# Performance work log

Hardware: AMD Instinct MI355X
Metric: run time of the kernel (lower is better)

## Reference

```python
import jax, jax.numpy as jnp
import numpy as np

B, S, D, C, H = 4, 2048, 1024, 2, 16
LN_EPS = 1e-5


def setup_inputs() -> dict:
    key = jax.random.key(0)
    ks = jax.random.split(key, 6)
    return {
        "token_emb": jax.random.normal(ks[0], (B, S, D), dtype=jnp.float32),
        "chunk_w": jax.random.normal(ks[1], (D, C * D), dtype=jnp.float32) * 0.02,
        "chunk_b": jnp.zeros((D,), dtype=jnp.float32),
        "in_proj_w": jax.random.normal(ks[2], (3 * D, D), dtype=jnp.float32) * 0.02,
        "in_proj_b": jnp.zeros((3 * D,), dtype=jnp.float32),
        "out_proj_w": jax.random.normal(ks[3], (D, D), dtype=jnp.float32) * 0.02,
        "out_proj_b": jnp.zeros((D,), dtype=jnp.float32),
        "ln_g": jnp.ones((D,), dtype=jnp.float32),
        "ln_b": jnp.zeros((D,), dtype=jnp.float32),
        "num_heads": H,
    }


def _layer_norm(x, g, b):
    mu = jnp.mean(x, axis=-1, keepdims=True)
    var = jnp.mean((x - mu) ** 2, axis=-1, keepdims=True)
    return (x - mu) * jax.lax.rsqrt(var + LN_EPS) * g + b


def reference(token_emb, chunk_w, chunk_b, in_proj_w, in_proj_b,
              out_proj_w, out_proj_b, ln_g, ln_b, num_heads):
    Bq, Sq, Dq = token_emb.shape
    c = chunk_w.shape[1] // Dq
    # Sliding windows with zero padding at the end (vectorized unfold).
    padded = jnp.pad(token_emb, ((0, 0), (0, c - 1), (0, 0)))
    # (B, S, c*D): concat the c shifted views along feature dim
    windows = jnp.concatenate([padded[:, k:k + Sq, :] for k in range(c)], axis=-1)
    chunk = jnp.einsum('bsf,df->bsd', windows, chunk_w) + chunk_b  # (B,S,D)

    # Multi-head self-attention (torch nn.MultiheadAttention semantics).
    qkv = jnp.einsum('bsd,ed->bse', chunk, in_proj_w) + in_proj_b
    q, k, v = jnp.split(qkv, 3, axis=-1)
    dh = Dq // num_heads
    q = q.reshape(Bq, Sq, num_heads, dh)
    k = k.reshape(Bq, Sq, num_heads, dh)
    v = v.reshape(Bq, Sq, num_heads, dh)
    scores = jnp.einsum('bqhd,bkhd->bhqk', q, k) / jnp.sqrt(jnp.float32(dh))
    probs = jax.nn.softmax(scores, axis=-1)
    attn = jnp.einsum('bhqk,bkhd->bqhd', probs, v).reshape(Bq, Sq, Dq)
    attn = jnp.einsum('bsd,ed->bse', attn, out_proj_w) + out_proj_b

    return _layer_norm(chunk + attn, ln_g, ln_b)
```

## Files before the change

kernel.cpp:

```cpp
#include <hip/hip_runtime.h>


typedef __bf16 bf16x8 __attribute__((ext_vector_type(8)));
typedef float f32x4 __attribute__((ext_vector_type(4)));
typedef float f32x16 __attribute__((ext_vector_type(16)));

#if __has_builtin(__builtin_amdgcn_exp2f)
#define EXP2(x) __builtin_amdgcn_exp2f(x)
#else
#define EXP2(x) exp2f(x)
#endif

__device__ __forceinline__ unsigned short f2bf(float x) {
  unsigned u = __float_as_uint(x);
  u += 0x7fffu + ((u >> 16) & 1u);
  return (unsigned short)(u >> 16);
}

__device__ __forceinline__ float bf2f(unsigned short x) {
  return __uint_as_float(((unsigned)x) << 16);
}

__device__ __forceinline__ void glds16(const ushort* g, ushort* l) {
  __builtin_amdgcn_global_load_lds(
      (const __attribute__((address_space(1))) unsigned int*)g,
      (__attribute__((address_space(3))) unsigned int*)l, 16, 0, 0);
}

__global__ __launch_bounds__(256) void build_awin(const float* __restrict__ emb,
                                                  ushort* __restrict__ aw) {
  const int i = blockIdx.x * 256 + threadIdx.x;
  const int e = i * 4;
  const int m = e >> 11;
  const int k = e & 2047;
  float4 v;
  if (k < 1024) {
    v = *(const float4*)(emb + (size_t)m * 1024 + k);
  } else {
    const int s = m & 2047;
    if (s == 2047) v = make_float4(0.f, 0.f, 0.f, 0.f);
    else           v = *(const float4*)(emb + (size_t)(m + 1) * 1024 + (k - 1024));
  }
  ushort4 o;
  o.x = f2bf(v.x); o.y = f2bf(v.y); o.z = f2bf(v.z); o.w = f2bf(v.w);
  *(ushort4*)(aw + (size_t)e) = o;
}

__global__ __launch_bounds__(256) void cvt_bf16(const float* __restrict__ in,
                                                ushort* __restrict__ out, int n4) {
  const int i = blockIdx.x * 256 + threadIdx.x;
  if (i >= n4) return;
  float4 v = ((const float4*)in)[i];
  ushort4 o;
  o.x = f2bf(v.x); o.y = f2bf(v.y); o.z = f2bf(v.z); o.w = f2bf(v.w);
  ((ushort4*)out)[i] = o;
}

template <int NT>
__global__ __launch_bounds__(256) void gemm_bt(
    const ushort* __restrict__ A, const ushort* __restrict__ W,
    const float* __restrict__ bias, int M, int N, int K, int mode,
    float* __restrict__ outf, ushort* __restrict__ outb,
    const ushort* __restrict__ residb) {
  constexpr int NTC = NT / 32;
  constexpr int BC  = NT / 32;
  __shared__ __align__(16) ushort sA[8192];
  __shared__ __align__(16) ushort sB[NT * 64];
  const int t = threadIdx.x, wave = t >> 6, lane = t & 63;
  const int c16 = lane & 15, quad = lane >> 4;
  const int wm = wave >> 1, wn = wave & 1;
  const int m0 = blockIdx.x * 128, n0 = blockIdx.y * NT;
  f32x4 acc[4][NTC] = {};
  const ushort* gA[4];
  const ushort* gB[BC];
  ushort* lA[4];
  ushort* lB[BC];
#pragma unroll
  for (int c = 0; c < 4; ++c) {
    const int j = wave * 4 + c;
    const int ks = j >> 1, row = (j & 1) * 64 + lane;
    gA[c] = A + (size_t)(m0 + row) * K + ks * 8;
    lA[c] = sA + j * 512;
  }
#pragma unroll
  for (int c = 0; c < BC; ++c) {
    const int j = wave * BC + c;
    int ksb, rowb;
    if (NT == 128) { ksb = j >> 1; rowb = (j & 1) * 64 + lane; }
    else           { ksb = j;      rowb = lane; }
    gB[c] = W + (size_t)(n0 + rowb) * K + ksb * 8;
    lB[c] = sB + j * 512;
  }
  for (int k0 = 0; k0 < K; k0 += 64) {
    __syncthreads();
#pragma unroll
    for (int c = 0; c < 4; ++c) glds16(gA[c] + k0, lA[c]);
#pragma unroll
    for (int c = 0; c < BC; ++c) glds16(gB[c] + k0, lB[c]);
    __syncthreads();
#pragma unroll
    for (int kc = 0; kc < 2; ++kc) {
      bf16x8 af[4], bfr[NTC];
#pragma unroll
      for (int i = 0; i < 4; ++i)
        af[i] = *(const bf16x8*)(sA + ((kc * 4 + quad) * 128 + wm * 64 + i * 16 + c16) * 8);
#pragma unroll
      for (int i = 0; i < NTC; ++i)
        bfr[i] = *(const bf16x8*)(sB + ((kc * 4 + quad) * NT + wn * (NT / 2) + i * 16 + c16) * 8);
#pragma unroll
      for (int mt = 0; mt < 4; ++mt)
#pragma unroll
        for (int nt = 0; nt < NTC; ++nt)
          acc[mt][nt] = __builtin_amdgcn_mfma_f32_16x16x32_bf16(af[mt], bfr[nt],
                                                                acc[mt][nt], 0, 0, 0);
    }
  }
  const float QS = 0.18033688011112042f;
  float bv[NTC];
#pragma unroll
  for (int nt = 0; nt < NTC; ++nt) bv[nt] = bias[n0 + wn * (NT / 2) + nt * 16 + c16];
#pragma unroll
  for (int mt = 0; mt < 4; ++mt) {
#pragma unroll
    for (int nt = 0; nt < NTC; ++nt) {
      const int n = n0 + wn * (NT / 2) + nt * 16 + c16;
#pragma unroll
      for (int r = 0; r < 4; ++r) {
        const int m = m0 + wm * 64 + mt * 16 + quad * 4 + r;
        const size_t idx = (size_t)m * N + n;
        float v = acc[mt][nt][r] + bv[nt];
        if (mode == 2)      { outf[idx] = v + bf2f(residb[idx]); }
        else {
          if (mode == 1 && n < 1024) v *= QS;
          outb[idx] = f2bf(v);
        }
      }
    }
  }
}

__global__ __launch_bounds__(256) void vtrans(const ushort* __restrict__ qkv,
                                              ushort* __restrict__ vt) {
  const int sb = blockIdx.x, h = blockIdx.y, b = blockIdx.z;
  __shared__ ushort tile[64][72];
  const int t = threadIdx.x;
  {
    const int row = t >> 3, c8 = (t & 7) * 8;
    const ushort* src = qkv + (size_t)(b * 2048 + sb * 64 + row) * 3072 + 2048 + h * 64 + c8;
    *(uint4*)&tile[row][c8]      = *(const uint4*)src;
    *(uint4*)&tile[row + 32][c8] = *(const uint4*)(src + 32 * 3072);
  }
  __syncthreads();
  const int d = t >> 2, seg = (t & 3) * 16;
  unsigned wbuf[8];
#pragma unroll
  for (int i = 0; i < 8; ++i)
    wbuf[i] = (unsigned)tile[seg + 2 * i][d] | ((unsigned)tile[seg + 2 * i + 1][d] << 16);
  ushort* dst = vt + (size_t)((b * 16 + h) * 64 + d) * 2048 + sb * 64 + seg;
  *(uint4*)(dst)     = *(uint4*)&wbuf[0];
  *(uint4*)(dst + 8) = *(uint4*)&wbuf[4];
}

__global__ __launch_bounds__(256, 4) void attn_kernel(
    const ushort* __restrict__ qkv, const ushort* __restrict__ vtp,
    ushort* __restrict__ attn_out) {
  const int S = 2048;
  const int bh = blockIdx.x, qblk = blockIdx.y;
  const int h = bh & 15, b = bh >> 4;
  const int t = threadIdx.x, wave = t >> 6, lane = t & 63;
  const int c32 = lane & 31, hi = lane >> 5;
  __shared__ __align__(16) ushort sK[8192];
  __shared__ __align__(16) ushort sV[8192];
  const int q0 = qblk * 128;
  const size_t qrow = (size_t)(b * S + q0 + wave * 32 + c32);
  const int swv0 = (c32 ^ (c32 >> 3)) & 15;
  const int dv1 = 32 + c32;
  const int swv1 = (dv1 ^ (dv1 >> 3)) & 15;
  bf16x8 qf[4];
  {
    const ushort* qp = qkv + qrow * 3072 + h * 64 + hi * 8;
#pragma unroll
    for (int dk = 0; dk < 4; ++dk) qf[dk] = *(const bf16x8*)(qp + dk * 16);
  }
  f32x16 o0 = {}, o1 = {};
  float li = 0.f;
  const int j0 = wave * 4;

  for (int kv0 = 0; kv0 < S; kv0 += 128) {
    __syncthreads();
#pragma unroll
    for (int c = 0; c < 4; ++c) {
      const int j = j0 + c;
      const int dslot = j >> 1, key = (j & 1) * 64 + lane;
      glds16(qkv + (size_t)(b * S + kv0 + key) * 3072 + 1024 + h * 64 + dslot * 8,
             sK + j * 512);
      const int d = j * 4 + (lane >> 4);
      const int ksv = (lane & 15) ^ ((d ^ (d >> 3)) & 15);
      glds16(vtp + (size_t)((b * 16 + h) * 64 + d) * S + kv0 + ksv * 8,
             sV + j * 512);
    }
    __syncthreads();
#pragma unroll
    for (int kt = 0; kt < 4; ++kt) {
      f32x16 z = {};
#pragma unroll
      for (int dk = 0; dk < 4; ++dk) {
        bf16x8 kf = *(const bf16x8*)(sK + ((dk * 2 + hi) * 128 + kt * 32 + c32) * 8);
        z = __builtin_amdgcn_mfma_f32_32x32x16_bf16(kf, qf[dk], z, 0, 0, 0);
      }
      uint2 w[4];
#pragma unroll
      for (int g = 0; g < 4; ++g) {
        const float p0 = EXP2(z[g * 4 + 0]);
        const float p1 = EXP2(z[g * 4 + 1]);
        const float p2 = EXP2(z[g * 4 + 2]);
        const float p3 = EXP2(z[g * 4 + 3]);
        li += (p0 + p1) + (p2 + p3);
        w[g].x = __builtin_amdgcn_perm(__float_as_uint(p1), __float_as_uint(p0),
                                       0x07060302u);
        w[g].y = __builtin_amdgcn_perm(__float_as_uint(p3), __float_as_uint(p2),
                                       0x07060302u);
      }
      uint2 pp[4];
#pragma unroll
      for (int g = 0; g < 4; ++g) {
        pp[g].x = __shfl_xor((int)w[g].x, 32);
        pp[g].y = __shfl_xor((int)w[g].y, 32);
      }
#pragma unroll
      for (int e = 0; e < 2; ++e) {
        const uint2 lo4 = hi ? pp[2 * e + 1] : w[2 * e];
        const uint2 hi4 = hi ? w[2 * e + 1] : pp[2 * e];
        const uint4 fr = make_uint4(lo4.x, lo4.y, hi4.x, hi4.y);
        bf16x8 pf;
        __builtin_memcpy(&pf, &fr, 16);
        const int ksl = kt * 4 + e * 2 + hi;
        bf16x8 vf0 = *(const bf16x8*)(sV + (c32 * 16 + (ksl ^ swv0)) * 8);
        o0 = __builtin_amdgcn_mfma_f32_32x32x16_bf16(vf0, pf, o0, 0, 0, 0);
        bf16x8 vf1 = *(const bf16x8*)(sV + (dv1 * 16 + (ksl ^ swv1)) * 8);
        o1 = __builtin_amdgcn_mfma_f32_32x32x16_bf16(vf1, pf, o1, 0, 0, 0);
      }
    }
  }
  li += __shfl_xor(li, 32);
  const float inv = 1.f / li;
  ushort* orow = attn_out + qrow * 1024 + h * 64;
#pragma unroll
  for (int dt = 0; dt < 2; ++dt) {
    const f32x16 ov = dt ? o1 : o0;
#pragma unroll
    for (int g = 0; g < 4; ++g) {
      float v0 = ov[g * 4 + 0] * inv, v1 = ov[g * 4 + 1] * inv;
      float v2 = ov[g * 4 + 2] * inv, v3 = ov[g * 4 + 3] * inv;
      uint2 w2;
      w2.x = (unsigned)f2bf(v0) | ((unsigned)f2bf(v1) << 16);
      w2.y = (unsigned)f2bf(v2) | ((unsigned)f2bf(v3) << 16);
      *(uint2*)(orow + dt * 32 + g * 8 + hi * 4) = w2;
    }
  }
}

__global__ __launch_bounds__(256) void ln_kernel(const float* __restrict__ y,
                                                 const float* __restrict__ g,
                                                 const float* __restrict__ bta,
                                                 float* __restrict__ out) {
  const int m = blockIdx.x;
  const int t = threadIdx.x;
  const float* row = y + (size_t)m * 1024;
  float4 v = ((const float4*)row)[t];
  float s = v.x + v.y + v.z + v.w;
  float s2 = v.x * v.x + v.y * v.y + v.z * v.z + v.w * v.w;
#pragma unroll
  for (int off = 1; off < 64; off <<= 1) {
    s += __shfl_xor(s, off, 64);
    s2 += __shfl_xor(s2, off, 64);
  }
  __shared__ float red[8];
  const int wave = t >> 6, lane = t & 63;
  if (lane == 0) { red[wave] = s; red[4 + wave] = s2; }
  __syncthreads();
  s = red[0] + red[1] + red[2] + red[3];
  s2 = red[4] + red[5] + red[6] + red[7];
  const float mu = s * (1.f / 1024.f);
  const float var = s2 * (1.f / 1024.f) - mu * mu;
  const float rs = rsqrtf(var + 1e-5f);
  float4 gg = ((const float4*)g)[t];
  float4 bb = ((const float4*)bta)[t];
  float4 o;
  o.x = (v.x - mu) * rs * gg.x + bb.x;
  o.y = (v.y - mu) * rs * gg.y + bb.y;
  o.z = (v.z - mu) * rs * gg.z + bb.z;
  o.w = (v.w - mu) * rs * gg.w + bb.w;
  ((float4*)(out + (size_t)m * 1024))[t] = o;
}

extern "C" void kernel_launch(void* const* d_in, const int* in_sizes, int n_in,
                              void* d_out, int out_size, void* d_ws, size_t ws_size,
                              hipStream_t stream) {
  const float* emb        = (const float*)d_in[0];
  const float* chunk_w    = (const float*)d_in[1];
  const float* chunk_b    = (const float*)d_in[2];
  const float* in_proj_w  = (const float*)d_in[3];
  const float* in_proj_b  = (const float*)d_in[4];
  const float* out_proj_w = (const float*)d_in[5];
  const float* out_proj_b = (const float*)d_in[6];
  const float* ln_g       = (const float*)d_in[7];
  const float* ln_b       = (const float*)d_in[8];

  char* w = (char*)d_ws;
  const size_t MBy = (size_t)1 << 20;
  ushort* qkvb   = (ushort*)(w + 0);
  ushort* awin   = (ushort*)(w + 0);
  float*  y      = (float*)(w + 0);
  ushort* chunkb = (ushort*)(w + 48 * MBy);
  ushort* vtb    = (ushort*)(w + 64 * MBy);
  ushort* attnb  = (ushort*)(w + 80 * MBy);
  ushort* cwb    = (ushort*)(w + 96 * MBy);
  ushort* ipwb   = (ushort*)(w + 100 * MBy);
  ushort* opwb   = (ushort*)(w + 106 * MBy);

  build_awin<<<16384, 256, 0, stream>>>(emb, awin);
  cvt_bf16<<<2048, 256, 0, stream>>>(chunk_w, cwb, 2 * 1024 * 1024 / 4);
  cvt_bf16<<<3072, 256, 0, stream>>>(in_proj_w, ipwb, 3 * 1024 * 1024 / 4);
  cvt_bf16<<<1024, 256, 0, stream>>>(out_proj_w, opwb, 1024 * 1024 / 4);

  gemm_bt<64><<<dim3(8192 / 128, 1024 / 64), 256, 0, stream>>>(
      awin, cwb, chunk_b, 8192, 1024, 2048, 0, nullptr, chunkb, nullptr);

  gemm_bt<128><<<dim3(8192 / 128, 3072 / 128), 256, 0, stream>>>(
      chunkb, ipwb, in_proj_b, 8192, 3072, 1024, 1, nullptr, qkvb, nullptr);

  vtrans<<<dim3(32, 16, 4), 256, 0, stream>>>(qkvb, vtb);

  attn_kernel<<<dim3(64, 2048 / 128, 1), 256, 0, stream>>>(qkvb, vtb, attnb);

  gemm_bt<64><<<dim3(8192 / 128, 1024 / 64), 256, 0, stream>>>(
      attnb, opwb, out_proj_b, 8192, 1024, 1024, 2, y, nullptr, chunkb);

  ln_kernel<<<8192, 256, 0, stream>>>(y, ln_g, ln_b, (float*)d_out);
}
```

Baseline: 491.3 us.

## Fuse sliding-window unfold into chunk GEMM and drop attention P shuffles

Instead of materialising a doubled-width bf16 window matrix, the embedding is converted once into a per-batch padded bf16 buffer with a zero row at the end of each batch. A dedicated chunk GEMM then loads one 129-row A tile and reads both the current row and the next row from shared memory, halving A-side traffic and removing the large intermediate write. The V-transpose kernel also reorders its stored key positions so that each lane's own softmax probabilities already form its PV MFMA fragment. That lets the attention kernel drop the cross-lane shuffles. The cost is a specialised kernel, an extra tiny zeroing launch, and a permuted V layout that the attention kernel depends on.

```diff
diff --git a/kernel.cpp b/kernel.cpp
--- a/kernel.cpp
+++ b/kernel.cpp
@@ -27,23 +27,22 @@
       (__attribute__((address_space(3))) unsigned int*)l, 16, 0, 0);
 }
 
-__global__ __launch_bounds__(256) void build_awin(const float* __restrict__ emb,
-                                                  ushort* __restrict__ aw) {
+__global__ __launch_bounds__(256) void cvt_emb(const float* __restrict__ emb,
+                                               ushort* __restrict__ embb) {
   const int i = blockIdx.x * 256 + threadIdx.x;
   const int e = i * 4;
-  const int m = e >> 11;
-  const int k = e & 2047;
-  float4 v;
-  if (k < 1024) {
-    v = *(const float4*)(emb + (size_t)m * 1024 + k);
-  } else {
-    const int s = m & 2047;
-    if (s == 2047) v = make_float4(0.f, 0.f, 0.f, 0.f);
-    else           v = *(const float4*)(emb + (size_t)(m + 1) * 1024 + (k - 1024));
-  }
+  const int m = e >> 10;
+  const int b = m >> 11, s = m & 2047;
+  float4 v = *(const float4*)(emb + (size_t)e);
   ushort4 o;
   o.x = f2bf(v.x); o.y = f2bf(v.y); o.z = f2bf(v.z); o.w = f2bf(v.w);
-  *(ushort4*)(aw + (size_t)e) = o;
+  *(ushort4*)(embb + ((size_t)(b * 2049 + s) << 10) + (e & 1023)) = o;
+}
+
+__global__ void zrow_kernel(ushort* __restrict__ embb) {
+  const int b = blockIdx.x, t = threadIdx.x;
+  ushort4 z = {0, 0, 0, 0};
+  *(ushort4*)(embb + ((size_t)(b * 2049 + 2048) << 10) + t * 4) = z;
 }
 
 __global__ __launch_bounds__(256) void cvt_bf16(const float* __restrict__ in,
@@ -54,6 +53,97 @@
   ushort4 o;
   o.x = f2bf(v.x); o.y = f2bf(v.y); o.z = f2bf(v.z); o.w = f2bf(v.w);
   ((ushort4*)out)[i] = o;
+}
+
+__global__ __launch_bounds__(256) void gemm_chunk(
+    const ushort* __restrict__ embb, const ushort* __restrict__ cwb,
+    const float* __restrict__ bias, ushort* __restrict__ outb) {
+  __shared__ __align__(16) ushort sA[8192];
+  __shared__ __align__(16) ushort sA2[512];
+  __shared__ __align__(16) ushort sB1[4096];
+  __shared__ __align__(16) ushort sB2[4096];
+  const int t = threadIdx.x, wave = t >> 6, lane = t & 63;
+  const int c16 = lane & 15, quad = lane >> 4;
+  const int wm = wave >> 1, wn = wave & 1;
+  const int m0 = blockIdx.x * 128, n0 = blockIdx.y * 64;
+  const int b = m0 >> 11, s0 = m0 & 2047;
+  const size_t rowbase = (size_t)(b * 2049 + s0);
+  f32x4 acc[4][2] = {};
+  const ushort* gA[4];
+  ushort* lA[4];
+#pragma unroll
+  for (int c = 0; c < 4; ++c) {
+    const int j = wave * 4 + c;
+    const int ks = j >> 1, row = (j & 1) * 64 + lane;
+    gA[c] = embb + ((rowbase + row) << 10) + ks * 8;
+    lA[c] = sA + j * 512;
+  }
+  const ushort* gA2 = embb + ((rowbase + 128) << 10) + (lane & 7) * 8;
+  const ushort* gB1[2];
+  const ushort* gB2[2];
+  ushort* lB1[2];
+  ushort* lB2[2];
+#pragma unroll
+  for (int c = 0; c < 2; ++c) {
+    const int j = wave * 2 + c;
+    gB1[c] = cwb + (size_t)(n0 + lane) * 2048 + j * 8;
+    gB2[c] = gB1[c] + 1024;
+    lB1[c] = sB1 + j * 512;
+    lB2[c] = sB2 + j * 512;
+  }
+  for (int k0 = 0; k0 < 1024; k0 += 64) {
+    __syncthreads();
+#pragma unroll
+    for (int c = 0; c < 4; ++c) glds16(gA[c] + k0, lA[c]);
+    if (wave == 3) glds16(gA2 + k0, sA2);
+#pragma unroll
+    for (int c = 0; c < 2; ++c) {
+      glds16(gB1[c] + k0, lB1[c]);
+      glds16(gB2[c] + k0, lB2[c]);
+    }
+    __syncthreads();
+#pragma unroll
+    for (int kc = 0; kc < 2; ++kc) {
+      const int ksl = kc * 4 + quad;
+      bf16x8 af1[4], af2[4], bf1[2], bf2[2];
+#pragma unroll
+      for (int i = 0; i < 4; ++i) {
+        const int row = wm * 64 + i * 16 + c16;
+        af1[i] = *(const bf16x8*)(sA + (ksl * 128 + row) * 8);
+        const ushort* p2 = (row + 1 < 128) ? (sA + (ksl * 128 + row + 1) * 8)
+                                           : (sA2 + ksl * 8);
+        af2[i] = *(const bf16x8*)p2;
+      }
+#pragma unroll
+      for (int i = 0; i < 2; ++i) {
+        bf1[i] = *(const bf16x8*)(sB1 + (ksl * 64 + wn * 32 + i * 16 + c16) * 8);
+        bf2[i] = *(const bf16x8*)(sB2 + (ksl * 64 + wn * 32 + i * 16 + c16) * 8);
+      }
+#pragma unroll
+      for (int mt = 0; mt < 4; ++mt)
+#pragma unroll
+        for (int nt = 0; nt < 2; ++nt) {
+          acc[mt][nt] = __builtin_amdgcn_mfma_f32_16x16x32_bf16(af1[mt], bf1[nt],
+                                                                acc[mt][nt], 0, 0, 0);
+          acc[mt][nt] = __builtin_amdgcn_mfma_f32_16x16x32_bf16(af2[mt], bf2[nt],
+                                                                acc[mt][nt], 0, 0, 0);
+        }
+    }
+  }
+  float bv[2];
+#pragma unroll
+  for (int nt = 0; nt < 2; ++nt) bv[nt] = bias[n0 + wn * 32 + nt * 16 + c16];
+#pragma unroll
+  for (int mt = 0; mt < 4; ++mt)
+#pragma unroll
+    for (int nt = 0; nt < 2; ++nt) {
+      const int n = n0 + wn * 32 + nt * 16 + c16;
+#pragma unroll
+      for (int r = 0; r < 4; ++r) {
+        const int m = m0 + wm * 64 + mt * 16 + quad * 4 + r;
+        outb[(size_t)m * 1024 + n] = f2bf(acc[mt][nt][r] + bv[nt]);
+      }
+    }
 }
 
 template <int NT>
@@ -131,7 +221,7 @@
         float v = acc[mt][nt][r] + bv[nt];
         if (mode == 2)      { outf[idx] = v + bf2f(residb[idx]); }
         else {
-          if (mode == 1 && n < 1024) v *= QS;
+          if (n < 1024) v *= QS;
           outb[idx] = f2bf(v);
         }
       }
@@ -157,8 +247,10 @@
   for (int i = 0; i < 8; ++i)
     wbuf[i] = (unsigned)tile[seg + 2 * i][d] | ((unsigned)tile[seg + 2 * i + 1][d] << 16);
   ushort* dst = vt + (size_t)((b * 16 + h) * 64 + d) * 2048 + sb * 64 + seg;
-  *(uint4*)(dst)     = *(uint4*)&wbuf[0];
-  *(uint4*)(dst + 8) = *(uint4*)&wbuf[4];
+  uint4 oA = make_uint4(wbuf[0], wbuf[1], wbuf[4], wbuf[5]);
+  uint4 oB = make_uint4(wbuf[2], wbuf[3], wbuf[6], wbuf[7]);
+  *(uint4*)(dst)     = oA;
+  *(uint4*)(dst + 8) = oB;
 }
 
 __global__ __launch_bounds__(256, 4) void attn_kernel(
@@ -221,20 +313,13 @@
         w[g].y = __builtin_amdgcn_perm(__float_as_uint(p3), __float_as_uint(p2),
                                        0x07060302u);
       }
-      uint2 pp[4];
-#pragma unroll
-      for (int g = 0; g < 4; ++g) {
-        pp[g].x = __shfl_xor((int)w[g].x, 32);
-        pp[g].y = __shfl_xor((int)w[g].y, 32);
-      }
-#pragma unroll
-      for (int e = 0; e < 2; ++e) {
-        const uint2 lo4 = hi ? pp[2 * e + 1] : w[2 * e];
-        const uint2 hi4 = hi ? w[2 * e + 1] : pp[2 * e];
-        const uint4 fr = make_uint4(lo4.x, lo4.y, hi4.x, hi4.y);
+#pragma unroll
+      for (int c = 0; c < 2; ++c) {
+        const uint4 fr = make_uint4(w[2 * c].x, w[2 * c].y,
+                                    w[2 * c + 1].x, w[2 * c + 1].y);
         bf16x8 pf;
         __builtin_memcpy(&pf, &fr, 16);
-        const int ksl = kt * 4 + e * 2 + hi;
+        const int ksl = kt * 4 + c * 2 + hi;
         bf16x8 vf0 = *(const bf16x8*)(sV + (c32 * 16 + (ksl ^ swv0)) * 8);
         o0 = __builtin_amdgcn_mfma_f32_32x32x16_bf16(vf0, pf, o0, 0, 0, 0);
         bf16x8 vf1 = *(const bf16x8*)(sV + (dv1 * 16 + (ksl ^ swv1)) * 8);
@@ -309,23 +394,24 @@
 
   char* w = (char*)d_ws;
   const size_t MBy = (size_t)1 << 20;
-  ushort* qkvb   = (ushort*)(w + 0);
-  ushort* awin   = (ushort*)(w + 0);
-  float*  y      = (float*)(w + 0);
-  ushort* chunkb = (ushort*)(w + 48 * MBy);
-  ushort* vtb    = (ushort*)(w + 64 * MBy);
-  ushort* attnb  = (ushort*)(w + 80 * MBy);
-  ushort* cwb    = (ushort*)(w + 96 * MBy);
-  ushort* ipwb   = (ushort*)(w + 100 * MBy);
-  ushort* opwb   = (ushort*)(w + 106 * MBy);
-
-  build_awin<<<16384, 256, 0, stream>>>(emb, awin);
+  ushort* embb   = (ushort*)(w + 0);
+  ushort* qkvb   = (ushort*)(w + 17 * MBy);
+  float*  y      = (float*)(w + 17 * MBy);
+  ushort* chunkb = (ushort*)(w + 65 * MBy);
+  ushort* vtb    = (ushort*)(w + 81 * MBy);
+  ushort* attnb  = (ushort*)(w + 97 * MBy);
+  ushort* cwb    = (ushort*)(w + 113 * MBy);
+  ushort* ipwb   = (ushort*)(w + 117 * MBy);
+  ushort* opwb   = (ushort*)(w + 123 * MBy);
+
+  cvt_emb<<<8192, 256, 0, stream>>>(emb, embb);
+  zrow_kernel<<<4, 256, 0, stream>>>(embb);
   cvt_bf16<<<2048, 256, 0, stream>>>(chunk_w, cwb, 2 * 1024 * 1024 / 4);
   cvt_bf16<<<3072, 256, 0, stream>>>(in_proj_w, ipwb, 3 * 1024 * 1024 / 4);
   cvt_bf16<<<1024, 256, 0, stream>>>(out_proj_w, opwb, 1024 * 1024 / 4);
 
-  gemm_bt<64><<<dim3(8192 / 128, 1024 / 64), 256, 0, stream>>>(
-      awin, cwb, chunk_b, 8192, 1024, 2048, 0, nullptr, chunkb, nullptr);
+  gemm_chunk<<<dim3(8192 / 128, 1024 / 64), 256, 0, stream>>>(
+      embb, cwb, chunk_b, chunkb);
 
   gemm_bt<128><<<dim3(8192 / 128, 3072 / 128), 256, 0, stream>>>(
       chunkb, ipwb, in_proj_b, 8192, 3072, 1024, 1, nullptr, qkvb, nullptr);
```

Result: faster. 455.8 us (-7.2%).
